# Performance work log

Measured on AMD Instinct MI355X. Metric: run time of the kernel, lower is better.

## Reference

```python
import jax, jax.numpy as jnp
import numpy as np

N_QUBITS = 12
DIM = 2 ** N_QUBITS  # 4096

_H = (jnp.array([[1.0, 1.0], [1.0, -1.0]]) / np.sqrt(2.0)).astype(jnp.complex64)
_X = jnp.array([[0.0, 1.0], [1.0, 0.0]], dtype=jnp.complex64)


def setup_inputs() -> dict:
    key = jax.random.key(0)
    k1, k2 = jax.random.split(key)
    state = jax.random.normal(k1, (8, 512, DIM), dtype=jnp.float32)
    params = jax.random.normal(k2, (N_QUBITS,), dtype=jnp.float32)
    return {"state": state, "params": params}


def _to_quantum(x):
    # faithful to _classical_to_quantum_inspired: normalize, phase = acos(|v|), sign * exp(i*phase)
    norms = jnp.linalg.norm(x, axis=-1, keepdims=True)
    v = x / (norms + 1e-8)
    mag = jnp.minimum(jnp.abs(v), 1.0)
    q = (jnp.sign(v) * jnp.exp(1j * jnp.arccos(mag))).astype(jnp.complex64)
    nrm = jnp.sqrt(jnp.sum(q.real ** 2 + q.imag ** 2, axis=-1, keepdims=True))
    return q / nrm.astype(jnp.complex64)


def _axis(q):
    # qubit q = bit q (LSB); tensor axes ordered MSB-first after batch axis 0
    return 1 + (N_QUBITS - 1 - q)


def _apply_1q(full, q, U):
    ax = _axis(q)
    moved = jnp.moveaxis(full, ax, -1)
    out = jnp.einsum('...b,ab->...a', moved, U)
    return jnp.moveaxis(out, -1, ax)


def _apply_ctrl(full, c, t, U):
    # apply U on target qubit t where control qubit c == 1
    axc = _axis(c)
    b0 = jnp.take(full, 0, axis=axc)
    b1 = jnp.take(full, 1, axis=axc)
    axt = _axis(t)
    axt_sub = axt - 1 if axt > axc else axt
    moved = jnp.moveaxis(b1, axt_sub, -1)
    b1n = jnp.moveaxis(jnp.einsum('...b,ab->...a', moved, U), -1, axt_sub)
    return jnp.stack([b0, b1n], axis=axc)


def _rx(theta):
    c = jnp.cos(theta / 2).astype(jnp.complex64)
    s = (-1j * jnp.sin(theta / 2)).astype(jnp.complex64)
    return jnp.stack([jnp.stack([c, s]), jnp.stack([s, c])])


def reference(state, params):
    B, T, D = state.shape
    psi = _to_quantum(state.reshape(B * T, D))  # (N, 2**n) complex64
    full = psi.reshape((B * T,) + (2,) * N_QUBITS)
    for q in range(N_QUBITS):
        full = _apply_1q(full, q, _H)                                  # Hadamard
        full = _apply_ctrl(full, q, (q + 1) % N_QUBITS, _rx(params[q]))  # controlled-RX
        if q < N_QUBITS - 1:
            full = _apply_ctrl(full, q, q + 1, _X)                     # CNOT
    amp = full.reshape(B * T, D)
    probs = amp.real ** 2 + amp.imag ** 2  # measurement probabilities
    return probs.reshape(B, T, D).astype(jnp.float32)
```

## Files before the change

kernel.cpp:

```cpp
#include <hip/hip_runtime.h>

#define NQ  12
#define DIM 4096
#define TPB 256

typedef float v2f __attribute__((ext_vector_type(2)));
typedef float v4f __attribute__((ext_vector_type(4)));


__device__ __forceinline__ float wave_reduce(float v) {
#pragma unroll
    for (int m = 32; m >= 1; m >>= 1) v += __shfl_xor(v, m, 64);
    return v;
}

#define BCAST(v, q) __uint_as_float(__builtin_amdgcn_readlane(__float_as_uint(v), (q)))

template <int MC, int MT, bool XGATE>
__device__ __forceinline__ void apply_layer(v2f* a, v2f ctv, v2f snv) {
#pragma unroll
    for (int i = 0; i < 16; ++i) {
        if (i & MC) continue;
        const int j = i | MC;
        const v2f t0 = a[i], t1 = a[j];
        a[i] = t0 + t1;
        a[j] = t0 - t1;
    }
#pragma unroll
    for (int i = 0; i < 16; ++i) {
        if (!(i & MC) || (i & MT)) continue;
        const int j = i | MT;
        const v2f b0 = a[i], b1 = a[j];
        const v2f s0 = snv * b0.yx;
        const v2f s1 = snv * b1.yx;
        if (XGATE) {
            a[i] = ctv * b1 + s0;
            a[j] = ctv * b0 + s1;
        } else {
            a[i] = ctv * b0 + s1;
            a[j] = ctv * b1 + s0;
        }
    }
}

__device__ __forceinline__ void st_pair(v2f* p, v2f lo, v2f hi) {
    v4f w; w.x = lo.x; w.y = lo.y; w.z = hi.x; w.w = hi.y;
    *(v4f*)p = w;
}
__device__ __forceinline__ void ld_pair(const v2f* p, v2f* lo, v2f* hi) {
    const v4f v = *(const v4f*)p;
    v2f q0; q0.x = v.x; q0.y = v.y;
    v2f q1; q1.x = v.z; q1.y = v.w;
    *lo = q0; *hi = q1;
}

__global__ __launch_bounds__(TPB, 4) void qlayer_kernel(
        const float* __restrict__ state, const float* __restrict__ params,
        float* __restrict__ out) {
    __shared__ __align__(16) v2f amp[4668];
    __shared__ float red[4];

    const int t = threadIdx.x;
    const int lane = t & 63;
    const long long sbase = (long long)blockIdx.x * DIM;

    const float th = params[lane < NQ ? lane : 0] * 0.5f;
    const float cl = cosf(th);
    const float sl = sinf(th);

    float x[16];
    const float4* gp = (const float4*)(state + sbase + t * 16);
    float ss = 0.f;
#pragma unroll
    for (int j = 0; j < 4; ++j) {
        const float4 v = gp[j];
        x[4 * j + 0] = v.x; x[4 * j + 1] = v.y;
        x[4 * j + 2] = v.z; x[4 * j + 3] = v.w;
        ss = fmaf(v.x, v.x, ss); ss = fmaf(v.y, v.y, ss);
        ss = fmaf(v.z, v.z, ss); ss = fmaf(v.w, v.w, ss);
    }
    ss = wave_reduce(ss);
    if (lane == 0) red[t >> 6] = ss;
    __syncthreads();
    const float nrm  = sqrtf(red[0] + red[1] + red[2] + red[3]);
    const float invd = 1.0f / (nrm + 1e-8f);

    v2f a[16];
#pragma unroll
    for (int k = 0; k < 16; ++k) {
        const float v   = x[k] * invd;
        const float re  = fminf(fmaxf(v, -1.0f), 1.0f);
        const float imb = sqrtf(fmaxf(1.0f - re * re, 0.f));
        const float im  = (v > 0.f) ? imb : ((v < 0.f) ? -imb : 0.f);
        v2f q; q.x = re; q.y = im;
        a[k] = q;
    }

#define CTV(q) ({ v2f _c; _c.x = BCAST(cl, q); _c.y = _c.x; _c; })
#define SNV(q) ({ float _s = BCAST(sl, q); v2f _v; _v.x = _s; _v.y = -_s; _v; })

    apply_layer<1, 2, true>(a, CTV(0), SNV(0));
    apply_layer<2, 4, true>(a, CTV(1), SNV(1));
    apply_layer<4, 8, true>(a, CTV(2), SNV(2));
    {
        v2f* wp = &amp[2 * (t & 7) + 146 * (t >> 3)];
#pragma unroll
        for (int k = 0; k < 8; ++k) st_pair(&wp[18 * k], a[k], a[k + 8]);
    }
    __syncthreads();

    {
        const v2f* rp = &amp[18 * (t & 7) + 146 * (t >> 3)];
#pragma unroll
        for (int m = 0; m < 8; ++m) ld_pair(&rp[2 * m], &a[2 * m], &a[2 * m + 1]);
    }
    apply_layer<1, 2, true>(a, CTV(3), SNV(3));
    apply_layer<2, 4, true>(a, CTV(4), SNV(4));
    apply_layer<4, 8, true>(a, CTV(5), SNV(5));
    __syncthreads();
    {
        v2f* wp = &amp[2 * ((t >> 3) & 7) + 146 * (t & 7) + 1168 * (t >> 6)];
#pragma unroll
        for (int k = 0; k < 8; ++k) st_pair(&wp[18 * k], a[k], a[k + 8]);
    }
    __syncthreads();

    {
        const v2f* rp = &amp[18 * (t & 7) + 146 * ((t >> 3) & 7) + 1168 * (t >> 6)];
#pragma unroll
        for (int m = 0; m < 8; ++m) ld_pair(&rp[2 * m], &a[2 * m], &a[2 * m + 1]);
    }
    apply_layer<1, 2, true>(a, CTV(6), SNV(6));
    apply_layer<2, 4, true>(a, CTV(7), SNV(7));
    apply_layer<4, 8, true>(a, CTV(8), SNV(8));
    __syncthreads();
    {
        v2f* wp = &amp[2 * (t >> 6) + 8 * ((t >> 3) & 1) + 146 * (t & 7)
                      + 1168 * ((t >> 4) & 3)];
#pragma unroll
        for (int k = 0; k < 8; ++k) st_pair(&wp[18 * k], a[k], a[k + 8]);
    }
    __syncthreads();

    {
        const v2f* rp = &amp[18 * (t >> 5) + 146 * (t & 7) + 1168 * ((t >> 3) & 3)];
#pragma unroll
        for (int m = 0; m < 8; ++m) ld_pair(&rp[2 * m], &a[2 * m], &a[2 * m + 1]);
    }
    apply_layer<1, 2, true >(a, CTV(9),  SNV(9));
    apply_layer<2, 4, true >(a, CTV(10), SNV(10));
    apply_layer<4, 8, false>(a, CTV(11), SNV(11));

    {
        const float scale = 0x1p-24f;
        float2* outp = (float2*)(out + sbase);
        const int obase = ((t >> 3) & 3) + 4 * (t & 7) + 32 * (t >> 5);
#pragma unroll
        for (int k = 0; k < 8; ++k) {
            const v2f q0 = a[k] * a[k];
            const v2f q1 = a[k | 8] * a[k | 8];
            outp[obase + (k << 8)] = make_float2((q0.x + q0.y) * scale,
                                                 (q1.x + q1.y) * scale);
        }
    }
#undef CTV
#undef SNV
}

extern "C" void kernel_launch(void* const* d_in, const int* in_sizes, int n_in,
                              void* d_out, int out_size, void* d_ws, size_t ws_size,
                              hipStream_t stream) {
    (void)in_sizes; (void)n_in; (void)out_size; (void)d_ws; (void)ws_size;
    const float* state  = (const float*)d_in[0];
    const float* params = (const float*)d_in[1];
    float* out = (float*)d_out;
    qlayer_kernel<<<dim3(4096), dim3(TPB), 0, stream>>>(state, params, out);
}
```

Measured before the change: 123.3 us.

## Process each state vector with one wavefront holding 64 amplitudes per lane

```diff
diff --git a/kernel.cpp b/kernel.cpp
--- a/kernel.cpp
+++ b/kernel.cpp
@@ -2,7 +2,6 @@
 
 #define NQ  12
 #define DIM 4096
-#define TPB 256
 
 typedef float v2f __attribute__((ext_vector_type(2)));
 typedef float v4f __attribute__((ext_vector_type(4)));
@@ -19,7 +18,7 @@
 template <int MC, int MT, bool XGATE>
 __device__ __forceinline__ void apply_layer(v2f* a, v2f ctv, v2f snv) {
 #pragma unroll
-    for (int i = 0; i < 16; ++i) {
+    for (int i = 0; i < 64; ++i) {
         if (i & MC) continue;
         const int j = i | MC;
         const v2f t0 = a[i], t1 = a[j];
@@ -27,7 +26,7 @@
         a[j] = t0 - t1;
     }
 #pragma unroll
-    for (int i = 0; i < 16; ++i) {
+    for (int i = 0; i < 64; ++i) {
         if (!(i & MC) || (i & MT)) continue;
         const int j = i | MT;
         const v2f b0 = a[i], b1 = a[j];
@@ -54,113 +53,92 @@
     *lo = q0; *hi = q1;
 }
 
-__global__ __launch_bounds__(TPB, 4) void qlayer_kernel(
+__global__ __launch_bounds__(64, 1) void qlayer_kernel(
         const float* __restrict__ state, const float* __restrict__ params,
         float* __restrict__ out) {
-    __shared__ __align__(16) v2f amp[4668];
-    __shared__ float red[4];
+    __shared__ __align__(16) v2f buf[64 * 66];
 
-    const int t = threadIdx.x;
-    const int lane = t & 63;
+    const int L = threadIdx.x;
     const long long sbase = (long long)blockIdx.x * DIM;
 
-    const float th = params[lane < NQ ? lane : 0] * 0.5f;
+    const float th = params[L < NQ ? L : 0] * 0.5f;
     const float cl = cosf(th);
     const float sl = sinf(th);
 
-    float x[16];
-    const float4* gp = (const float4*)(state + sbase + t * 16);
+    v4f xv[16];
+    const v4f* gp = (const v4f*)(state + sbase + L * 64);
     float ss = 0.f;
 #pragma unroll
-    for (int j = 0; j < 4; ++j) {
-        const float4 v = gp[j];
-        x[4 * j + 0] = v.x; x[4 * j + 1] = v.y;
-        x[4 * j + 2] = v.z; x[4 * j + 3] = v.w;
-        ss = fmaf(v.x, v.x, ss); ss = fmaf(v.y, v.y, ss);
-        ss = fmaf(v.z, v.z, ss); ss = fmaf(v.w, v.w, ss);
+    for (int i = 0; i < 16; ++i) {
+        xv[i] = gp[i];
+        ss = fmaf(xv[i].x, xv[i].x, ss); ss = fmaf(xv[i].y, xv[i].y, ss);
+        ss = fmaf(xv[i].z, xv[i].z, ss); ss = fmaf(xv[i].w, xv[i].w, ss);
     }
     ss = wave_reduce(ss);
-    if (lane == 0) red[t >> 6] = ss;
-    __syncthreads();
-    const float nrm  = sqrtf(red[0] + red[1] + red[2] + red[3]);
-    const float invd = 1.0f / (nrm + 1e-8f);
+    const float invd = 1.0f / (sqrtf(ss) + 1e-8f);
 
-    v2f a[16];
+    v2f a[64];
 #pragma unroll
-    for (int k = 0; k < 16; ++k) {
-        const float v   = x[k] * invd;
-        const float re  = fminf(fmaxf(v, -1.0f), 1.0f);
-        const float imb = sqrtf(fmaxf(1.0f - re * re, 0.f));
-        const float im  = (v > 0.f) ? imb : ((v < 0.f) ? -imb : 0.f);
-        v2f q; q.x = re; q.y = im;
-        a[k] = q;
+    for (int i = 0; i < 16; ++i) {
+#pragma unroll
+        for (int u = 0; u < 4; ++u) {
+            const float v   = xv[i][u] * invd;
+            const float re  = fminf(fmaxf(v, -1.0f), 1.0f);
+            const float imb = sqrtf(fmaxf(1.0f - re * re, 0.f));
+            const float im  = (v > 0.f) ? imb : ((v < 0.f) ? -imb : 0.f);
+            v2f q; q.x = re; q.y = im;
+            a[4 * i + u] = q;
+        }
     }
 
 #define CTV(q) ({ v2f _c; _c.x = BCAST(cl, q); _c.y = _c.x; _c; })
 #define SNV(q) ({ float _s = BCAST(sl, q); v2f _v; _v.x = _s; _v.y = -_s; _v; })
 
-    apply_layer<1, 2, true>(a, CTV(0), SNV(0));
-    apply_layer<2, 4, true>(a, CTV(1), SNV(1));
-    apply_layer<4, 8, true>(a, CTV(2), SNV(2));
-    {
-        v2f* wp = &amp[2 * (t & 7) + 146 * (t >> 3)];
+    const int wb = 2 * (L & 31) + 66 * (L >> 5);
+
+    apply_layer< 1,  2, true>(a, CTV(0), SNV(0));
+    apply_layer< 2,  4, true>(a, CTV(1), SNV(1));
+    apply_layer< 4,  8, true>(a, CTV(2), SNV(2));
+    apply_layer< 8, 16, true>(a, CTV(3), SNV(3));
+    apply_layer<16, 32, true>(a, CTV(4), SNV(4));
 #pragma unroll
-        for (int k = 0; k < 8; ++k) st_pair(&wp[18 * k], a[k], a[k + 8]);
-    }
-    __syncthreads();
+    for (int r = 0; r < 32; ++r)
+        st_pair(&buf[wb + 132 * r], a[r], a[r + 32]);
 
-    {
-        const v2f* rp = &amp[18 * (t & 7) + 146 * (t >> 3)];
 #pragma unroll
-        for (int m = 0; m < 8; ++m) ld_pair(&rp[2 * m], &a[2 * m], &a[2 * m + 1]);
-    }
-    apply_layer<1, 2, true>(a, CTV(3), SNV(3));
-    apply_layer<2, 4, true>(a, CTV(4), SNV(4));
-    apply_layer<4, 8, true>(a, CTV(5), SNV(5));
-    __syncthreads();
-    {
-        v2f* wp = &amp[2 * ((t >> 3) & 7) + 146 * (t & 7) + 1168 * (t >> 6)];
+    for (int m = 0; m < 32; ++m)
+        ld_pair(&buf[66 * L + 2 * m], &a[2 * m], &a[2 * m + 1]);
+
+    apply_layer< 1,  2, true>(a, CTV(5), SNV(5));
+    apply_layer< 2,  4, true>(a, CTV(6), SNV(6));
+    apply_layer< 4,  8, true>(a, CTV(7), SNV(7));
+    apply_layer< 8, 16, true>(a, CTV(8), SNV(8));
+    apply_layer<16, 32, true>(a, CTV(9), SNV(9));
 #pragma unroll
-        for (int k = 0; k < 8; ++k) st_pair(&wp[18 * k], a[k], a[k + 8]);
-    }
-    __syncthreads();
+    for (int r = 0; r < 32; ++r)
+        st_pair(&buf[wb + 132 * r], a[r], a[r + 32]);
 
-    {
-        const v2f* rp = &amp[18 * (t & 7) + 146 * ((t >> 3) & 7) + 1168 * (t >> 6)];
 #pragma unroll
-        for (int m = 0; m < 8; ++m) ld_pair(&rp[2 * m], &a[2 * m], &a[2 * m + 1]);
-    }
-    apply_layer<1, 2, true>(a, CTV(6), SNV(6));
-    apply_layer<2, 4, true>(a, CTV(7), SNV(7));
-    apply_layer<4, 8, true>(a, CTV(8), SNV(8));
-    __syncthreads();
-    {
-        v2f* wp = &amp[2 * (t >> 6) + 8 * ((t >> 3) & 1) + 146 * (t & 7)
-                      + 1168 * ((t >> 4) & 3)];
+    for (int m = 0; m < 32; ++m)
+        ld_pair(&buf[66 * L + 2 * m], &a[2 * m], &a[2 * m + 1]);
+
+    apply_layer<1, 2, true >(a, CTV(10), SNV(10));
+    apply_layer<2, 4, false>(a, CTV(11), SNV(11));
+
+    const float scale = 0x1p-24f;
+    float* op = out + sbase + 16 * L;
 #pragma unroll
-        for (int k = 0; k < 8; ++k) st_pair(&wp[18 * k], a[k], a[k + 8]);
-    }
-    __syncthreads();
-
-    {
-        const v2f* rp = &amp[18 * (t >> 5) + 146 * (t & 7) + 1168 * ((t >> 3) & 3)];
+    for (int c = 0; c < 4; ++c) {
 #pragma unroll
-        for (int m = 0; m < 8; ++m) ld_pair(&rp[2 * m], &a[2 * m], &a[2 * m + 1]);
-    }
-    apply_layer<1, 2, true >(a, CTV(9),  SNV(9));
-    apply_layer<2, 4, true >(a, CTV(10), SNV(10));
-    apply_layer<4, 8, false>(a, CTV(11), SNV(11));
-
-    {
-        const float scale = 0x1p-24f;
-        float2* outp = (float2*)(out + sbase);
-        const int obase = ((t >> 3) & 3) + 4 * (t & 7) + 32 * (t >> 5);
+        for (int j = 0; j < 4; ++j) {
+            v4f w;
 #pragma unroll
-        for (int k = 0; k < 8; ++k) {
-            const v2f q0 = a[k] * a[k];
-            const v2f q1 = a[k | 8] * a[k | 8];
-            outp[obase + (k << 8)] = make_float2((q0.x + q0.y) * scale,
-                                                 (q1.x + q1.y) * scale);
+            for (int u = 0; u < 4; ++u) {
+                const v2f z = a[c + 16 * j + 4 * u];
+                const v2f q = z * z;
+                w[u] = (q.x + q.y) * scale;
+            }
+            *(v4f*)(op + 1024 * c + 4 * j) = w;
         }
     }
 #undef CTV
@@ -174,5 +152,5 @@
     const float* state  = (const float*)d_in[0];
     const float* params = (const float*)d_in[1];
     float* out = (float*)d_out;
-    qlayer_kernel<<<dim3(4096), dim3(TPB), 0, stream>>>(state, params, out);
+    qlayer_kernel<<<dim3(4096), dim3(64), 0, stream>>>(state, params, out);
 }
```

After: 151.1 us. 1.23x slower.
